# Optimization experiments

Measured on AMD Instinct MI355X. Metric: run time of the kernel, lower is better.

Reference implementation:

```python
import jax, jax.numpy as jnp
import numpy as np

N_HEAD = 16
HEAD_DIM = 64
HIDDEN = 1024
ROPE_BASE = 10000.0


def _rope_tables(L, d):
    # inv_freq over even indices, emb = concat([freqs, freqs]) -> [L, d]
    inv_freq = 1.0 / (ROPE_BASE ** (jnp.arange(0, d, 2, dtype=jnp.float32) / d))
    freqs = jnp.arange(L, dtype=jnp.float32)[:, None] * inv_freq[None, :]  # [L, d/2]
    emb = jnp.concatenate([freqs, freqs], axis=-1)  # [L, d]
    return jnp.cos(emb), jnp.sin(emb)


def _rotate_half(t):
    d2 = t.shape[-1] // 2
    return jnp.concatenate([-t[..., d2:], t[..., :d2]], axis=-1)


def setup_inputs() -> dict:
    key = jax.random.key(0)
    ks = jax.random.split(key, 5)
    B, L = 1, 4096
    x = jax.random.normal(ks[0], (B, L, HIDDEN), dtype=jnp.float32)
    sc = 1.0 / np.sqrt(HIDDEN)
    wq = jax.random.normal(ks[1], (HIDDEN, HIDDEN), dtype=jnp.float32) * sc
    wk = jax.random.normal(ks[2], (HIDDEN, HIDDEN), dtype=jnp.float32) * sc
    wv = jax.random.normal(ks[3], (HIDDEN, HIDDEN), dtype=jnp.float32) * sc
    wo = jax.random.normal(ks[4], (HIDDEN, HIDDEN), dtype=jnp.float32) * sc
    return {"x": x, "wq": wq, "wk": wk, "wv": wv, "wo": wo}


def reference(x, wq, wk, wv, wo):
    B, L, D = x.shape
    H, Hd = N_HEAD, HEAD_DIM
    # projections (torch Linear: y = x @ W^T), split heads -> [B, H, L, Hd]
    q = jnp.einsum('bld,ed->ble', x, wq).reshape(B, L, H, Hd).transpose(0, 2, 1, 3)
    k = jnp.einsum('bld,ed->ble', x, wk).reshape(B, L, H, Hd).transpose(0, 2, 1, 3)
    v = jnp.einsum('bld,ed->ble', x, wv).reshape(B, L, H, Hd).transpose(0, 2, 1, 3)
    cos, sin = _rope_tables(L, Hd)  # [L, Hd]
    q = q * cos[None, None] + _rotate_half(q) * sin[None, None]
    k = k * cos[None, None] + _rotate_half(k) * sin[None, None]
    # causal SDPA, scale = 1/sqrt(head_dim)
    scores = jnp.einsum('bhqd,bhkd->bhqk', q, k) / jnp.sqrt(jnp.float32(Hd))
    causal = jnp.tril(jnp.ones((L, L), dtype=bool))
    scores = jnp.where(causal[None, None], scores, jnp.finfo(scores.dtype).min)
    attn = jax.nn.softmax(scores, axis=-1)
    out = jnp.einsum('bhqk,bhkd->bhqd', attn, v)  # [B, H, L, Hd]
    out = out.transpose(0, 2, 1, 3).reshape(B, L, D)
    return jnp.einsum('bld,ed->ble', out, wo)
```

## Files before the change

### kernel.cpp

```cpp
#include <hip/hip_runtime.h>
#include <math.h>
#include <type_traits>

constexpr int DM = 1024;
constexpr int NH = 16;
constexpr int HD = 64;
constexpr int LDQ = 3072;
constexpr int SPLIT_ST = 38;
constexpr int PENT = 4224;

typedef __attribute__((ext_vector_type(8))) short bf16x8;
typedef __attribute__((ext_vector_type(4))) float f32x4;

__device__ __forceinline__ unsigned short f2bf(float f) {
    union { float f; unsigned u; } v; v.f = f;
    unsigned r = v.u + 0x7FFFu + ((v.u >> 16) & 1u);
    return (unsigned short)(r >> 16);
}
__device__ __forceinline__ float bf2f(unsigned short h) {
    union { unsigned u; float f; } v; v.u = ((unsigned)h) << 16;
    return v.f;
}
__device__ __forceinline__ void gload16(const unsigned short* g, unsigned short* lds) {
    __builtin_amdgcn_global_load_lds(
        (const __attribute__((address_space(1))) unsigned int*)g,
        (__attribute__((address_space(3))) unsigned int*)lds, 16, 0, 0);
}
__device__ __forceinline__ unsigned cvt_pk_bf16(float lo, float hi) {
    unsigned r;
    asm("v_cvt_pk_bf16_f32 %0, %1, %2" : "=v"(r) : "v"(lo), "v"(hi));
    return r;
}
#define MFMA_BF16(a, b, c) __builtin_amdgcn_mfma_f32_16x16x32_bf16(a, b, c, 0, 0, 0)

__device__ __forceinline__ bf16x8 pack_swap(const f32x4& s0, const f32x4& s1) {
    unsigned c00 = cvt_pk_bf16(s0[0], s0[1]);
    unsigned c01 = cvt_pk_bf16(s0[2], s0[3]);
    unsigned c10 = cvt_pk_bf16(s1[0], s1[1]);
    unsigned c11 = cvt_pk_bf16(s1[2], s1[3]);
    asm("v_permlane32_swap_b32 %0, %1" : "+v"(c00), "+v"(c10));
    asm("v_permlane16_swap_b32 %0, %1" : "+v"(c00), "+v"(c10));
    asm("v_permlane32_swap_b32 %0, %1" : "+v"(c01), "+v"(c11));
    asm("v_permlane16_swap_b32 %0, %1" : "+v"(c01), "+v"(c11));
    union { unsigned u[4]; bf16x8 b; } r;
    r.u[0] = c00; r.u[1] = c01; r.u[2] = c10; r.u[3] = c11;
    return r.b;
}

__global__ __launch_bounds__(256)
void convert_bf16(const float* __restrict__ x, const float* __restrict__ wq,
                  const float* __restrict__ wk, const float* __restrict__ wv,
                  const float* __restrict__ wo, unsigned short* __restrict__ dst,
                  long long xElems) {
    const long long W = (long long)DM * DM;
    long long base = ((long long)blockIdx.x * 256 + threadIdx.x) * 8;
    const float* src; long long off;
    if (base < xElems) { src = x; off = base; }
    else {
        long long r = base - xElems;
        int wi = (int)(r / W); off = r - (long long)wi * W;
        src = wi == 0 ? wq : wi == 1 ? wk : wi == 2 ? wv : wo;
    }
    float4 a = *reinterpret_cast<const float4*>(src + off);
    float4 b = *reinterpret_cast<const float4*>(src + off + 4);
    uint4 o;
    o.x = (unsigned)f2bf(a.x) | ((unsigned)f2bf(a.y) << 16);
    o.y = (unsigned)f2bf(a.z) | ((unsigned)f2bf(a.w) << 16);
    o.z = (unsigned)f2bf(b.x) | ((unsigned)f2bf(b.y) << 16);
    o.w = (unsigned)f2bf(b.z) | ((unsigned)f2bf(b.w) << 16);
    *reinterpret_cast<uint4*>(dst + base) = o;
}

template <typename OT>
__global__ __launch_bounds__(256)
void gemm_bf16(const unsigned short* __restrict__ A, const unsigned short* __restrict__ B,
               OT* __restrict__ C, int M, int N, int K) {
    constexpr int BK = 32;
    __shared__ unsigned short As[128 * BK];
    __shared__ unsigned short Bs[128 * BK];
    const int t = threadIdx.x;
    const int w = t >> 6, l = t & 63;
    const int lg = l >> 4, ln = l & 15;

    const int nx = gridDim.x;
    const int nwg = gridDim.x * gridDim.y;
    int wg = blockIdx.y * nx + blockIdx.x;
    wg = (wg & 7) * (nwg >> 3) + (wg >> 3);
    const int bm = (wg / nx) * 128, bn = (wg % nx) * 128;
    const int wr = (w >> 1) * 64, wc = (w & 1) * 64;

    const int li0 = t, li1 = 256 + t;
    const int r0 = li0 >> 2, c0 = (li0 & 3) ^ ((r0 >> 1) & 3);
    const int r1 = li1 >> 2, c1 = (li1 & 3) ^ ((r1 >> 1) & 3);
    const unsigned short* gA0 = A + (size_t)(bm + r0) * K + c0 * 8;
    const unsigned short* gA1 = A + (size_t)(bm + r1) * K + c1 * 8;
    const unsigned short* gB0 = B + (size_t)(bn + r0) * K + c0 * 8;
    const unsigned short* gB1 = B + (size_t)(bn + r1) * K + c1 * 8;
    unsigned short* lA0 = As + (size_t)(w * 64) * 8;
    unsigned short* lA1 = As + (size_t)(256 + w * 64) * 8;
    unsigned short* lB0 = Bs + (size_t)(w * 64) * 8;
    unsigned short* lB1 = Bs + (size_t)(256 + w * 64) * 8;

    int aoff[4], boff[4];
#pragma unroll
    for (int m = 0; m < 4; ++m) { int R = wr + m * 16 + ln; aoff[m] = R * 64 + ((lg ^ ((R >> 1) & 3)) * 16); }
#pragma unroll
    for (int n = 0; n < 4; ++n) { int R = wc + n * 16 + ln; boff[n] = R * 64 + ((lg ^ ((R >> 1) & 3)) * 16); }

    const f32x4 z4 = {0.f, 0.f, 0.f, 0.f};
    f32x4 acc[4][4];
#pragma unroll
    for (int m = 0; m < 4; ++m)
#pragma unroll
        for (int n = 0; n < 4; ++n) acc[m][n] = z4;

    for (int k0 = 0; k0 < K; k0 += BK) {
        __syncthreads();
        gload16(gA0 + k0, lA0);
        gload16(gA1 + k0, lA1);
        gload16(gB0 + k0, lB0);
        gload16(gB1 + k0, lB1);
        __syncthreads();
        bf16x8 af[4], bfr[4];
#pragma unroll
        for (int m = 0; m < 4; ++m) af[m] = *(const bf16x8*)((const char*)As + aoff[m]);
#pragma unroll
        for (int n = 0; n < 4; ++n) bfr[n] = *(const bf16x8*)((const char*)Bs + boff[n]);
#pragma unroll
        for (int m = 0; m < 4; ++m)
#pragma unroll
            for (int n = 0; n < 4; ++n)
                acc[m][n] = MFMA_BF16(af[m], bfr[n], acc[m][n]);
    }

#pragma unroll
    for (int m = 0; m < 4; ++m)
#pragma unroll
        for (int n = 0; n < 4; ++n)
#pragma unroll
            for (int rg = 0; rg < 4; ++rg) {
                int row = bm + wr + m * 16 + lg * 4 + rg;
                int col = bn + wc + n * 16 + ln;
                if constexpr (std::is_same<OT, float>::value)
                    C[(size_t)row * N + col] = acc[m][n][rg];
                else
                    C[(size_t)row * N + col] = f2bf(acc[m][n][rg]);
            }
}

__global__ __launch_bounds__(512)
void rope_bf16(unsigned short* __restrict__ qkv) {
    constexpr float SCQ = 0.18033688011112042f;
    const int l = blockIdx.x;
    const int j = threadIdx.x & 31, h = threadIdx.x >> 5;
    const float inv = exp2f(-(float)j * (13.287712379549449f / 32.0f));
    const float ang = (float)l * inv;
    float s, c;
    sincosf(ang, &s, &c);
    const size_t base = (size_t)l * LDQ + h * HD + j;
    float a = bf2f(qkv[base]), b = bf2f(qkv[base + 32]);
    qkv[base]      = f2bf((a * c - b * s) * SCQ);
    qkv[base + 32] = f2bf((b * c + a * s) * SCQ);
    a = bf2f(qkv[base + DM]); b = bf2f(qkv[base + DM + 32]);
    qkv[base + DM]      = f2bf(a * c - b * s);
    qkv[base + DM + 32] = f2bf(b * c + a * s);
}

__global__ __launch_bounds__(256)
void transp_v(const unsigned short* __restrict__ qkv, unsigned short* __restrict__ vt,
              int L) {
    __shared__ unsigned LT[64][33];
    const int l0 = blockIdx.x * 64;
    const int h = blockIdx.y;
    const int t = threadIdx.x;
    const int jj = t >> 3;
    const int dc = t & 7;
    const unsigned short* vrow = qkv + 2 * DM + (size_t)(l0 + 2 * jj) * LDQ + h * HD + dc * 8;
    uint4 a = *reinterpret_cast<const uint4*>(vrow);
    uint4 b = *reinterpret_cast<const uint4*>(vrow + LDQ);
    const unsigned aw[4] = {a.x, a.y, a.z, a.w};
    const unsigned bw[4] = {b.x, b.y, b.z, b.w};
#pragma unroll
    for (int e = 0; e < 4; ++e) {
        LT[dc * 8 + e * 2][jj]     = __builtin_amdgcn_perm(bw[e], aw[e], 0x05040100u);
        LT[dc * 8 + e * 2 + 1][jj] = __builtin_amdgcn_perm(bw[e], aw[e], 0x07060302u);
    }
    __syncthreads();
#pragma unroll
    for (int it = 0; it < 2; ++it) {
        const int aidx = it * 256 + t;
        const int d = aidx >> 3, c = aidx & 7;
        uint4 o;
        o.x = LT[d][c * 4];     o.y = LT[d][c * 4 + 1];
        o.z = LT[d][c * 4 + 2]; o.w = LT[d][c * 4 + 3];
        *reinterpret_cast<uint4*>(vt + ((size_t)h * 64 + d) * L + l0 + c * 8) = o;
    }
}

__global__ __launch_bounds__(256)
void attn_mfma(const unsigned short* __restrict__ qkv,
               const unsigned short* __restrict__ vt,
               unsigned short* __restrict__ ob,
               float* __restrict__ pbuf, int L) {
    __shared__ unsigned short Ks[4096];
    __shared__ unsigned short Vs[4096];
    __shared__ unsigned short Ps[32 * 72];

    const int bid = blockIdx.x;
    const int xcd = bid & 7, rest = bid >> 3;
    const int h = xcd + 8 * (rest & 1);
    const int j = rest >> 1;
    int st, klo, khi;
    if (j < 6)       { st = 37 - j;        klo = 0;  khi = st + 1; }
    else if (j < 32) { st = 38 + (j - 6);  klo = 0;  khi = 32; }
    else if (j < 58) { st = 63 - (j - 32); klo = 32; khi = st + 1; }
    else             { st = 31 - (j - 58); klo = 0;  khi = st + 1; }
    const bool partial = (j >= 6 && j < 58);
    const int part = (j < 32) ? 0 : 1;
    const int q0 = st * 64;

    const int t = threadIdx.x, w = t >> 6, l = t & 63;
    const int lg = l >> 4, ln = l & 15;

    const unsigned short* kc[2];
    const unsigned short* vc[2];
    int ldso[2];
#pragma unroll
    for (int i = 0; i < 2; ++i) {
        const int pc = t + 256 * i;
        const int r = pc >> 3, cc = (pc & 7) ^ (r & 7);
        kc[i] = qkv + DM + (size_t)(klo * 64 + r) * LDQ + h * HD + cc * 8;
        vc[i] = vt + ((size_t)h * 64 + r) * L + klo * 64 + cc * 8;
        ldso[i] = pc * 8;
    }

    int foff[4][2];
#pragma unroll
    for (int n = 0; n < 4; ++n)
#pragma unroll
        for (int ks = 0; ks < 2; ++ks) {
            const int R = n * 16 + ln;
            foff[n][ks] = R * 128 + (((ks * 4 + lg) ^ (R & 7)) * 16);
        }
    const int prow2 = ((w & 1) * 16 + ln) * 144;

    const f32x4 z4 = {0.f, 0.f, 0.f, 0.f};

    bf16x8 qf[2];
#pragma unroll
    for (int ks = 0; ks < 2; ++ks)
        qf[ks] = *reinterpret_cast<const bf16x8*>(
            qkv + (size_t)(q0 + w * 16 + ln) * LDQ + h * HD + ks * 32 + lg * 8);

    f32x4 oa[4];
#pragma unroll
    for (int dn = 0; dn < 4; ++dn) oa[dn] = z4;
    float m_i = -INFINITY, l_i = 0.f;

    for (int kt = klo; kt < khi; ++kt) {
        const int kv0 = kt * 64;

#pragma unroll
        for (int i = 0; i < 2; ++i) gload16(kc[i], Ks + ldso[i]);
#pragma unroll
        for (int i = 0; i < 2; ++i) gload16(vc[i], Vs + ldso[i]);
#pragma unroll
        for (int i = 0; i < 2; ++i) { kc[i] += (size_t)64 * LDQ; vc[i] += 64; }
        __syncthreads();

        bf16x8 kf[4][2];
#pragma unroll
        for (int n = 0; n < 4; ++n)
#pragma unroll
            for (int ks = 0; ks < 2; ++ks)
                kf[n][ks] = *reinterpret_cast<const bf16x8*>((const char*)Ks + foff[n][ks]);
        f32x4 s[4];
        __builtin_amdgcn_s_setprio(1);
#pragma unroll
        for (int n = 0; n < 4; ++n) {
            f32x4 acc = MFMA_BF16(kf[n][0], qf[0], z4);
            s[n] = MFMA_BF16(kf[n][1], qf[1], acc);
        }
        __builtin_amdgcn_s_setprio(0);

        if (kv0 + 63 > q0 + w * 16) {
            const int qq = q0 + w * 16 + ln;
#pragma unroll
            for (int n = 0; n < 4; ++n)
#pragma unroll
                for (int rg = 0; rg < 4; ++rg)
                    if (kv0 + n * 16 + lg * 4 + rg > qq) s[n][rg] = -INFINITY;
        }

        float mx = fmaxf(fmaxf(s[0][0], s[0][1]), fmaxf(s[0][2], s[0][3]));
#pragma unroll
        for (int n = 1; n < 4; ++n)
            mx = fmaxf(mx, fmaxf(fmaxf(s[n][0], s[n][1]),
                                 fmaxf(s[n][2], s[n][3])));
        mx = fmaxf(mx, __shfl_xor(mx, 16));
        mx = fmaxf(mx, __shfl_xor(mx, 32));
        if (__any(mx > m_i + 8.f)) {
            const float mn = fmaxf(m_i, mx);
            const float sc = exp2f(m_i - mn);
            m_i = mn;
            l_i *= sc;
#pragma unroll
            for (int dn = 0; dn < 4; ++dn) oa[dn] *= sc;
        }
        float ps = 0.f;
#pragma unroll
        for (int n = 0; n < 4; ++n)
#pragma unroll
            for (int rg = 0; rg < 4; ++rg) {
                const float pv = __builtin_amdgcn_exp2f(s[n][rg] - m_i);
                s[n][rg] = pv;
                ps += pv;
            }
        ps += __shfl_xor(ps, 16);
        ps += __shfl_xor(ps, 32);
        l_i += ps;

        bf16x8 pf0 = pack_swap(s[0], s[1]);
        bf16x8 pf1 = pack_swap(s[2], s[3]);

        bf16x8 vf[4][2];
#pragma unroll
        for (int dn = 0; dn < 4; ++dn)
#pragma unroll
            for (int ks = 0; ks < 2; ++ks)
                vf[dn][ks] = *reinterpret_cast<const bf16x8*>((const char*)Vs + foff[dn][ks]);
        __builtin_amdgcn_s_setprio(1);
#pragma unroll
        for (int dn = 0; dn < 4; ++dn) {
            oa[dn] = MFMA_BF16(vf[dn][0], pf0, oa[dn]);
            oa[dn] = MFMA_BF16(vf[dn][1], pf1, oa[dn]);
        }
        __builtin_amdgcn_s_setprio(0);

        __syncthreads();
    }

    if (partial) {
        const int sidx = st - SPLIT_ST;
        float* pb = pbuf + (size_t)((sidx * NH + h) * 2 + part) * PENT;
        const int q = w * 16 + ln;
#pragma unroll
        for (int dn = 0; dn < 4; ++dn)
            *reinterpret_cast<f32x4*>(pb + q * 64 + dn * 16 + lg * 4) = oa[dn];
        if (lg == 0) {
            pb[4096 + q] = m_i;
            pb[4160 + q] = l_i;
        }
    } else {
        const float inv = 1.f / l_i;
        uint2 orow[4];
#pragma unroll
        for (int dn = 0; dn < 4; ++dn) {
            f32x4 o = oa[dn] * inv;
            orow[dn] = make_uint2(cvt_pk_bf16(o[0], o[1]), cvt_pk_bf16(o[2], o[3]));
        }
#pragma unroll
        for (int half = 0; half < 2; ++half) {
            if ((w >> 1) == half) {
#pragma unroll
                for (int dn = 0; dn < 4; ++dn)
                    *reinterpret_cast<uint2*>((char*)Ps + prow2 + dn * 32 + lg * 8) =
                        orow[dn];
            }
            __syncthreads();
            {
                const int r = t >> 3, c = (t & 7) * 8;
                const bf16x8 vv =
                    *reinterpret_cast<const bf16x8*>((const char*)Ps + r * 144 + c * 2);
                *reinterpret_cast<bf16x8*>(
                    ob + (size_t)(q0 + half * 32 + r) * DM + h * HD + c) = vv;
            }
            __syncthreads();
        }
    }
}

__global__ __launch_bounds__(256)
void combine_split(const float* __restrict__ pbuf, unsigned short* __restrict__ ob) {
    const int sidx = blockIdx.x, h = blockIdx.y;
    const float* p0 = pbuf + (size_t)((sidx * NH + h) * 2 + 0) * PENT;
    const float* p1 = pbuf + (size_t)((sidx * NH + h) * 2 + 1) * PENT;
    const int t = threadIdx.x;
    const int q = t >> 2, dg = (t & 3) * 16;
    const float m1 = p0[4096 + q], l1 = p0[4160 + q];
    const float m2 = p1[4096 + q], l2 = p1[4160 + q];
    const float m = fmaxf(m1, m2);
    const float w1 = exp2f(m1 - m), w2 = exp2f(m2 - m);
    const float inv = 1.f / (w1 * l1 + w2 * l2);
    const int q0 = (sidx + SPLIT_ST) * 64;
#pragma unroll
    for (int e = 0; e < 4; ++e) {
        f32x4 a = *reinterpret_cast<const f32x4*>(p0 + q * 64 + dg + e * 4);
        f32x4 b = *reinterpret_cast<const f32x4*>(p1 + q * 64 + dg + e * 4);
        f32x4 o = (a * w1 + b * w2) * inv;
        *reinterpret_cast<uint2*>(ob + (size_t)(q0 + q) * DM + h * HD + dg + e * 4) =
            make_uint2(cvt_pk_bf16(o[0], o[1]), cvt_pk_bf16(o[2], o[3]));
    }
}

extern "C" void kernel_launch(void* const* d_in, const int* in_sizes, int n_in,
                              void* d_out, int out_size, void* d_ws, size_t ws_size,
                              hipStream_t stream) {
    const float* x  = (const float*)d_in[0];
    const float* wq = (const float*)d_in[1];
    const float* wk = (const float*)d_in[2];
    const float* wv = (const float*)d_in[3];
    const float* wo = (const float*)d_in[4];

    const int L = in_sizes[0] / DM;
    const size_t NE = (size_t)L * DM;
    const size_t W  = (size_t)DM * DM;

    unsigned short* xb   = (unsigned short*)d_ws;
    unsigned short* wqb  = xb + NE;
    unsigned short* wob  = wqb + 3 * W;
    unsigned short* qkvb = wob + W;
    unsigned short* ab   = qkvb + (size_t)L * LDQ;
    unsigned short* vtb  = (unsigned short*)d_out;
    float* pbuf = (float*)d_ws;

    const long long totalConv = (long long)(NE + 4 * W);
    convert_bf16<<<dim3((unsigned)(totalConv / 8 / 256)), dim3(256), 0, stream>>>(
        x, wq, wk, wv, wo, xb, (long long)NE);

    gemm_bf16<unsigned short><<<dim3(LDQ / 128, L / 128), dim3(256), 0, stream>>>(
        xb, wqb, qkvb, L, LDQ, DM);

    rope_bf16<<<dim3(L), dim3(512), 0, stream>>>(qkvb);

    transp_v<<<dim3(L / 64, NH), dim3(256), 0, stream>>>(qkvb, vtb, L);

    attn_mfma<<<dim3(90 * NH), dim3(256), 0, stream>>>(qkvb, vtb, ab, pbuf, L);

    combine_split<<<dim3(64 - SPLIT_ST, NH), dim3(256), 0, stream>>>(pbuf, ab);

    gemm_bf16<float><<<dim3(DM / 128, L / 128), dim3(256), 0, stream>>>(
        ab, wob, (float*)d_out, L, DM, DM);
}
```

Before: 155.5 us.

## Process two 64-key tiles per attention loop iteration with doubled LDS buffers

The flash-attention loop now loads two consecutive K/V tiles (128 keys) into doubled shared-memory buffers per iteration and runs one online-softmax update across both. This halves the number of barriers and max/rescale reductions per key and gives the MFMA units more independent work between syncs. A tail path handles an odd leftover tile. In exchange, LDS use per block roughly doubles and register pressure rises, which may reduce occupancy.

```diff
diff --git a/kernel.cpp b/kernel.cpp
--- a/kernel.cpp
+++ b/kernel.cpp
@@ -202,8 +202,8 @@
                const unsigned short* __restrict__ vt,
                unsigned short* __restrict__ ob,
                float* __restrict__ pbuf, int L) {
-    __shared__ unsigned short Ks[4096];
-    __shared__ unsigned short Vs[4096];
+    __shared__ unsigned short Ks[2 * 4096];
+    __shared__ unsigned short Vs[2 * 4096];
     __shared__ unsigned short Ps[32 * 72];
 
     const int bid = blockIdx.x;
@@ -222,15 +222,15 @@
     const int t = threadIdx.x, w = t >> 6, l = t & 63;
     const int lg = l >> 4, ln = l & 15;
 
-    const unsigned short* kc[2];
-    const unsigned short* vc[2];
-    int ldso[2];
-#pragma unroll
-    for (int i = 0; i < 2; ++i) {
+    const unsigned short* kc[4];
+    const unsigned short* vc[4];
+    int ldso[4];
+#pragma unroll
+    for (int i = 0; i < 4; ++i) {
         const int pc = t + 256 * i;
         const int r = pc >> 3, cc = (pc & 7) ^ (r & 7);
         kc[i] = qkv + DM + (size_t)(klo * 64 + r) * LDQ + h * HD + cc * 8;
-        vc[i] = vt + ((size_t)h * 64 + r) * L + klo * 64 + cc * 8;
+        vc[i] = vt + ((size_t)h * 64 + (r & 63)) * L + klo * 64 + (r >> 6) * 64 + cc * 8;
         ldso[i] = pc * 8;
     }
 
@@ -257,39 +257,123 @@
     for (int dn = 0; dn < 4; ++dn) oa[dn] = z4;
     float m_i = -INFINITY, l_i = 0.f;
 
-    for (int kt = klo; kt < khi; ++kt) {
+    const int qrow = q0 + w * 16 + ln;
+
+    int kt = klo;
+    for (; kt + 2 <= khi; kt += 2) {
         const int kv0 = kt * 64;
 
 #pragma unroll
+        for (int i = 0; i < 4; ++i) gload16(kc[i], Ks + ldso[i]);
+#pragma unroll
+        for (int i = 0; i < 4; ++i) gload16(vc[i], Vs + ldso[i]);
+#pragma unroll
+        for (int i = 0; i < 4; ++i) { kc[i] += (size_t)128 * LDQ; vc[i] += 128; }
+        __syncthreads();
+
+        f32x4 s[2][4];
+        __builtin_amdgcn_s_setprio(1);
+#pragma unroll
+        for (int ts = 0; ts < 2; ++ts) {
+            const char* KsB = (const char*)Ks + ts * 8192;
+#pragma unroll
+            for (int n = 0; n < 4; ++n) {
+                bf16x8 k0 = *reinterpret_cast<const bf16x8*>(KsB + foff[n][0]);
+                bf16x8 k1 = *reinterpret_cast<const bf16x8*>(KsB + foff[n][1]);
+                f32x4 acc = MFMA_BF16(k0, qf[0], z4);
+                s[ts][n] = MFMA_BF16(k1, qf[1], acc);
+            }
+        }
+        __builtin_amdgcn_s_setprio(0);
+
+#pragma unroll
+        for (int ts = 0; ts < 2; ++ts) {
+            const int kv0t = kv0 + ts * 64;
+            if (kv0t + 63 > q0 + w * 16) {
+#pragma unroll
+                for (int n = 0; n < 4; ++n)
+#pragma unroll
+                    for (int rg = 0; rg < 4; ++rg)
+                        if (kv0t + n * 16 + lg * 4 + rg > qrow) s[ts][n][rg] = -INFINITY;
+            }
+        }
+
+        float mx = -INFINITY;
+#pragma unroll
+        for (int ts = 0; ts < 2; ++ts)
+#pragma unroll
+            for (int n = 0; n < 4; ++n)
+                mx = fmaxf(mx, fmaxf(fmaxf(s[ts][n][0], s[ts][n][1]),
+                                     fmaxf(s[ts][n][2], s[ts][n][3])));
+        mx = fmaxf(mx, __shfl_xor(mx, 16));
+        mx = fmaxf(mx, __shfl_xor(mx, 32));
+        if (__any(mx > m_i + 8.f)) {
+            const float mn = fmaxf(m_i, mx);
+            const float sc = exp2f(m_i - mn);
+            m_i = mn;
+            l_i *= sc;
+#pragma unroll
+            for (int dn = 0; dn < 4; ++dn) oa[dn] *= sc;
+        }
+        float ps = 0.f;
+#pragma unroll
+        for (int ts = 0; ts < 2; ++ts)
+#pragma unroll
+            for (int n = 0; n < 4; ++n)
+#pragma unroll
+                for (int rg = 0; rg < 4; ++rg) {
+                    const float pv = __builtin_amdgcn_exp2f(s[ts][n][rg] - m_i);
+                    s[ts][n][rg] = pv;
+                    ps += pv;
+                }
+        ps += __shfl_xor(ps, 16);
+        ps += __shfl_xor(ps, 32);
+        l_i += ps;
+
+        __builtin_amdgcn_s_setprio(1);
+#pragma unroll
+        for (int ts = 0; ts < 2; ++ts) {
+            bf16x8 pf0 = pack_swap(s[ts][0], s[ts][1]);
+            bf16x8 pf1 = pack_swap(s[ts][2], s[ts][3]);
+            const char* VsB = (const char*)Vs + ts * 8192;
+#pragma unroll
+            for (int dn = 0; dn < 4; ++dn) {
+                bf16x8 v0 = *reinterpret_cast<const bf16x8*>(VsB + foff[dn][0]);
+                bf16x8 v1 = *reinterpret_cast<const bf16x8*>(VsB + foff[dn][1]);
+                oa[dn] = MFMA_BF16(v0, pf0, oa[dn]);
+                oa[dn] = MFMA_BF16(v1, pf1, oa[dn]);
+            }
+        }
+        __builtin_amdgcn_s_setprio(0);
+
+        __syncthreads();
+    }
+
+    if (kt < khi) {
+        const int kv0 = kt * 64;
+#pragma unroll
         for (int i = 0; i < 2; ++i) gload16(kc[i], Ks + ldso[i]);
 #pragma unroll
         for (int i = 0; i < 2; ++i) gload16(vc[i], Vs + ldso[i]);
-#pragma unroll
-        for (int i = 0; i < 2; ++i) { kc[i] += (size_t)64 * LDQ; vc[i] += 64; }
         __syncthreads();
 
-        bf16x8 kf[4][2];
-#pragma unroll
-        for (int n = 0; n < 4; ++n)
-#pragma unroll
-            for (int ks = 0; ks < 2; ++ks)
-                kf[n][ks] = *reinterpret_cast<const bf16x8*>((const char*)Ks + foff[n][ks]);
         f32x4 s[4];
         __builtin_amdgcn_s_setprio(1);
 #pragma unroll
         for (int n = 0; n < 4; ++n) {
-            f32x4 acc = MFMA_BF16(kf[n][0], qf[0], z4);
-            s[n] = MFMA_BF16(kf[n][1], qf[1], acc);
+            bf16x8 k0 = *reinterpret_cast<const bf16x8*>((const char*)Ks + foff[n][0]);
+            bf16x8 k1 = *reinterpret_cast<const bf16x8*>((const char*)Ks + foff[n][1]);
+            f32x4 acc = MFMA_BF16(k0, qf[0], z4);
+            s[n] = MFMA_BF16(k1, qf[1], acc);
         }
         __builtin_amdgcn_s_setprio(0);
 
         if (kv0 + 63 > q0 + w * 16) {
-            const int qq = q0 + w * 16 + ln;
 #pragma unroll
             for (int n = 0; n < 4; ++n)
 #pragma unroll
                 for (int rg = 0; rg < 4; ++rg)
-                    if (kv0 + n * 16 + lg * 4 + rg > qq) s[n][rg] = -INFINITY;
+                    if (kv0 + n * 16 + lg * 4 + rg > qrow) s[n][rg] = -INFINITY;
         }
 
         float mx = fmaxf(fmaxf(s[0][0], s[0][1]), fmaxf(s[0][2], s[0][3]));
@@ -322,21 +406,15 @@
 
         bf16x8 pf0 = pack_swap(s[0], s[1]);
         bf16x8 pf1 = pack_swap(s[2], s[3]);
-
-        bf16x8 vf[4][2];
-#pragma unroll
-        for (int dn = 0; dn < 4; ++dn)
-#pragma unroll
-            for (int ks = 0; ks < 2; ++ks)
-                vf[dn][ks] = *reinterpret_cast<const bf16x8*>((const char*)Vs + foff[dn][ks]);
         __builtin_amdgcn_s_setprio(1);
 #pragma unroll
         for (int dn = 0; dn < 4; ++dn) {
-            oa[dn] = MFMA_BF16(vf[dn][0], pf0, oa[dn]);
-            oa[dn] = MFMA_BF16(vf[dn][1], pf1, oa[dn]);
+            bf16x8 v0 = *reinterpret_cast<const bf16x8*>((const char*)Vs + foff[dn][0]);
+            bf16x8 v1 = *reinterpret_cast<const bf16x8*>((const char*)Vs + foff[dn][1]);
+            oa[dn] = MFMA_BF16(v0, pf0, oa[dn]);
+            oa[dn] = MFMA_BF16(v1, pf1, oa[dn]);
         }
         __builtin_amdgcn_s_setprio(0);
-
         __syncthreads();
     }
 
```

Measured after the change: 159.2 us. 1.02x slower.
